# Optimization experiments

Measured on AMD Instinct MI355X. Metric: run time of the kernel, lower is better.

## Reference

```python
import jax, jax.numpy as jnp
import numpy as np

NUM_TOKENS = 100
D_MODEL = 256
NUM_RBF = 50
CUTOFF = 12.0


def setup_inputs() -> dict:
    key = jax.random.key(0)
    k1, k2, k3, k4, k5 = jax.random.split(key, 5)
    B, N = 16, 512
    atomic_numbers = jax.random.randint(k1, (B, N), 0, NUM_TOKENS)
    # scale positions so pairwise distances span [0, cutoff]
    positions = jax.random.normal(k2, (B, N, 3), dtype=jnp.float32) * 3.0
    token_emb = jax.random.normal(k3, (NUM_TOKENS, D_MODEL), dtype=jnp.float32) * 0.02
    proj_w = jax.random.normal(k4, (NUM_RBF, D_MODEL), dtype=jnp.float32) * (1.0 / np.sqrt(NUM_RBF))
    proj_b = jax.random.normal(k5, (D_MODEL,), dtype=jnp.float32) * 0.01
    return {"atomic_numbers": atomic_numbers, "positions": positions,
            "token_emb": token_emb, "proj_w": proj_w, "proj_b": proj_b}


def reference(atomic_numbers, positions, token_emb, proj_w, proj_b):
    # pairwise distances [B, N, N]
    diff = positions[:, :, None, :] - positions[:, None, :, :]
    dist = jnp.sqrt(jnp.sum(diff * diff, axis=-1) + 1e-8)
    # fixed Gaussian RBF expansion [B, N, N, K]
    centers = jnp.linspace(0.0, CUTOFF, NUM_RBF, dtype=jnp.float32)
    width = (centers[1] - centers[0]) * 2.0
    rbf = jnp.exp(-((dist[..., None] - centers) ** 2) / (width * width))
    # mean over neighbor axis -> [B, N, K]
    rbf_mean = jnp.mean(rbf, axis=2)
    rbf_embeddings = rbf_mean @ proj_w + proj_b  # [B, N, d_model]
    token_embeddings = token_emb[atomic_numbers]  # [B, N, d_model]
    return token_embeddings + rbf_embeddings
```

## Files before the change

### kernel.cpp

```cpp
#include <hip/hip_runtime.h>

#define S_C     2.45229158f
#define TWO_DS  1.20112241f

typedef float v2f __attribute__((ext_vector_type(2)));

__device__ __forceinline__ float fast_exp2(float x) {
#if __has_builtin(__builtin_amdgcn_exp2f)
    return __builtin_amdgcn_exp2f(x);
#else
    float r;
    asm("v_exp_f32 %0, %1" : "=v"(r) : "v"(x));
    return r;
#endif
}
__device__ __forceinline__ float fast_sqrt(float x) {
#if __has_builtin(__builtin_amdgcn_sqrtf)
    return __builtin_amdgcn_sqrtf(x);
#else
    return sqrtf(x);
#endif
}

__constant__ const float NEGC[5] = {0.0f, -6.00561204f, -12.0112241f, -18.0168361f, -24.0224482f};
#define E5_1 6.73794700e-3f
#define E5_2 4.53999298e-5f
#define E5_3 3.05902321e-7f
#define E5_4 2.06115362e-9f
#define E10_1 4.53999298e-5f
#define E10_2 2.06115362e-9f
#define E10_3 9.35762297e-14f
#define E10_4 4.24835426e-18f

template <bool FUSED>
__global__ __launch_bounds__(256)
void rbf_mean_kernel(const float* __restrict__ pos,
                     float* __restrict__ meanout,
                     const int* __restrict__ an,
                     const float* __restrict__ te,
                     const float* __restrict__ pw,
                     const float* __restrict__ pb,
                     float* __restrict__ out)
{
    __shared__ v2f red2[4][32 * 25];
    __shared__ float ms[4][52];

    const int w    = threadIdx.x >> 6;
    const int lane = threadIdx.x & 63;
    const int row  = blockIdx.x * 4 + w;
    const int b    = row >> 9;
    const int i    = row & 511;

    const float* posb = pos + (size_t)b * 512 * 3;

    float jx[8], jy[8], jz[8];
#pragma unroll
    for (int jj = 0; jj < 8; ++jj) {
        const int j = jj * 64 + lane;
        jx[jj] = posb[j * 3 + 0];
        jy[jj] = posb[j * 3 + 1];
        jz[jj] = posb[j * 3 + 2];
    }
    const float pix = posb[i * 3 + 0];
    const float piy = posb[i * 3 + 1];
    const float piz = posb[i * 3 + 2];

    v2f acc[25];
#pragma unroll
    for (int m = 0; m < 25; ++m) acc[m] = (v2f){0.0f, 0.0f};

#pragma unroll
    for (int jj = 0; jj < 8; ++jj) {
        const float dx = pix - jx[jj];
        const float dy = piy - jy[jj];
        const float dz = piz - jz[jj];
        const float d2 = fmaf(dx, dx, fmaf(dy, dy, fmaf(dz, dz, 1e-8f)));
        float dS = fast_sqrt(d2) * S_C;
        dS = fminf(dS, 42.0f);
        const float Ap = fast_exp2(dS * TWO_DS);
        const float A  = Ap * Ap;

#pragma unroll
        for (int c = 0; c < 5; ++c) {
            const float u  = dS + NEGC[c];
            const float t0 = fast_exp2(-(u * u));
            const float Ac  = (c == 0) ? Ap :
                              (c == 1) ? Ap * E5_1 :
                              (c == 2) ? Ap * E5_2 :
                              (c == 3) ? Ap * E5_3 : Ap * E5_4;
            const float Ac2 = (c == 0) ? A :
                              (c == 1) ? A * E10_1 :
                              (c == 2) ? A * E10_2 :
                              (c == 3) ? A * E10_3 : A * E10_4;
            v2f g = {t0, t0 * Ac};
            acc[5 * c + 0] += g;
            const v2f M = {Ac2, Ac2};
#pragma unroll
            for (int t = 1; t < 5; ++t) {
                g = g * M;
                acc[5 * c + t] += g;
            }
        }
    }

    {
        const v2f QP[5] = {{1.0f,            0.778800783f},
                           {0.367879441f,    0.105399225f},
                           {1.83156389e-2f,  1.93045414e-3f},
                           {1.23409804e-4f,  4.78511739e-6f},
                           {1.12535175e-7f,  1.60522806e-9f}};
#pragma unroll
        for (int m = 0; m < 25; ++m) acc[m] = acc[m] * QP[m % 5];
    }

#pragma unroll
    for (int m = 0; m < 25; ++m) {
        const float lx = __shfl_xor(acc[m].x, 1);
        const float ly = __shfl_xor(acc[m].y, 1);
        acc[m] += (v2f){lx, ly};
    }
    if ((lane & 1) == 0) {
        v2f* myrow = &red2[w][(lane >> 1) * 25];
#pragma unroll
        for (int m = 0; m < 25; ++m) myrow[m] = acc[m];
    }
    __syncthreads();

    float meanv = 0.0f;
    if (lane < 50) {
        const float* col = (const float*)&red2[w][0] + lane;
        float s0 = 0.f, s1 = 0.f, s2 = 0.f, s3 = 0.f;
#pragma unroll
        for (int r = 0; r < 32; r += 4) {
            s0 += col[(r + 0) * 50];
            s1 += col[(r + 1) * 50];
            s2 += col[(r + 2) * 50];
            s3 += col[(r + 3) * 50];
        }
        meanv = ((s0 + s1) + (s2 + s3)) * (1.0f / 512.0f);
    }

    if (!FUSED) {
        if (lane < 50) meanout[(size_t)row * 50 + lane] = meanv;
        return;
    }

    if (lane < 50) ms[w][lane] = meanv;
    __syncthreads();

    const int tok = an[row];
    float4 o = reinterpret_cast<const float4*>(pb)[lane];
    const float4 t = reinterpret_cast<const float4*>(te + (size_t)tok * 256)[lane];
    o.x += t.x; o.y += t.y; o.z += t.z; o.w += t.w;
#pragma unroll
    for (int k = 0; k < 50; ++k) {
        const float mk = ms[w][k];
        const float4 w4 = reinterpret_cast<const float4*>(pw + k * 256)[lane];
        o.x = fmaf(mk, w4.x, o.x);
        o.y = fmaf(mk, w4.y, o.y);
        o.z = fmaf(mk, w4.z, o.z);
        o.w = fmaf(mk, w4.w, o.w);
    }
    reinterpret_cast<float4*>(out)[(size_t)row * 64 + lane] = o;
}

__global__ __launch_bounds__(256)
void proj_kernel(const float* __restrict__ mean,
                 const int* __restrict__ an,
                 const float* __restrict__ te,
                 const float* __restrict__ pw,
                 const float* __restrict__ pb,
                 float* __restrict__ out)
{
    const int w    = threadIdx.x >> 6;
    const int lane = threadIdx.x & 63;
    int wid = blockIdx.x * 4 + w;
    wid = __builtin_amdgcn_readfirstlane(wid);
    const int row0 = wid * 4;

    const float4 bias = reinterpret_cast<const float4*>(pb)[lane];
    float4 o[4];
#pragma unroll
    for (int r = 0; r < 4; ++r) {
        const int tok = an[row0 + r];
        const float4 t = reinterpret_cast<const float4*>(te + (size_t)tok * 256)[lane];
        o[r].x = bias.x + t.x; o[r].y = bias.y + t.y;
        o[r].z = bias.z + t.z; o[r].w = bias.w + t.w;
    }
#pragma unroll
    for (int k = 0; k < 50; ++k) {
        const float4 w4 = reinterpret_cast<const float4*>(pw + (size_t)k * 256)[lane];
#pragma unroll
        for (int r = 0; r < 4; ++r) {
            const float mk = mean[(size_t)(row0 + r) * 50 + k];
            o[r].x = fmaf(mk, w4.x, o[r].x);
            o[r].y = fmaf(mk, w4.y, o[r].y);
            o[r].z = fmaf(mk, w4.z, o[r].z);
            o[r].w = fmaf(mk, w4.w, o[r].w);
        }
    }
#pragma unroll
    for (int r = 0; r < 4; ++r)
        reinterpret_cast<float4*>(out)[(size_t)(row0 + r) * 64 + lane] = o[r];
}

extern "C" void kernel_launch(void* const* d_in, const int* in_sizes, int n_in,
                              void* d_out, int out_size, void* d_ws, size_t ws_size,
                              hipStream_t stream)
{
    const int*   an  = (const int*)  d_in[0];
    const float* pos = (const float*)d_in[1];
    const float* te  = (const float*)d_in[2];
    const float* pw  = (const float*)d_in[3];
    const float* pb  = (const float*)d_in[4];
    float* out = (float*)d_out;

    const size_t mean_bytes = (size_t)8192 * 50 * sizeof(float);
    if (ws_size >= mean_bytes) {
        float* mean = (float*)d_ws;
        rbf_mean_kernel<false><<<2048, 256, 0, stream>>>(pos, mean, nullptr, nullptr,
                                                         nullptr, nullptr, nullptr);
        proj_kernel<<<512, 256, 0, stream>>>(mean, an, te, pw, pb, out);
    } else {
        rbf_mean_kernel<true><<<2048, 256, 0, stream>>>(pos, nullptr, an, te, pw, pb, out);
    }
}
```

Before: 26.64 us.

## Always run single fused RBF-mean and projection kernel, drop block barriers

Removes the two-kernel path, where means were written to workspace and a separate projection kernel read them back, and always launches one fused kernel that does the RBF mean and the projection together. This avoids a second launch and the global-memory round trip for the means. The cost is that the projection weights are reloaded for every row instead of being shared across four rows. Both __syncthreads are removed because each wave only uses its own shared-memory slice, which relies on wavefront lockstep for LDS ordering. The constant-memory NEGC table and the squared-exponent constants are replaced with inline arithmetic.

```diff
diff --git a/kernel.cpp b/kernel.cpp
--- a/kernel.cpp
+++ b/kernel.cpp
@@ -2,6 +2,11 @@
 
 #define S_C     2.45229158f
 #define TWO_DS  1.20112241f
+#define TEN_D   6.00560980f
+#define E5_1 6.73794700e-3f
+#define E5_2 4.53999298e-5f
+#define E5_3 3.05902321e-7f
+#define E5_4 2.06115362e-9f
 
 typedef float v2f __attribute__((ext_vector_type(2)));
 
@@ -22,27 +27,15 @@
 #endif
 }
 
-__constant__ const float NEGC[5] = {0.0f, -6.00561204f, -12.0112241f, -18.0168361f, -24.0224482f};
-#define E5_1 6.73794700e-3f
-#define E5_2 4.53999298e-5f
-#define E5_3 3.05902321e-7f
-#define E5_4 2.06115362e-9f
-#define E10_1 4.53999298e-5f
-#define E10_2 2.06115362e-9f
-#define E10_3 9.35762297e-14f
-#define E10_4 4.24835426e-18f
-
-template <bool FUSED>
 __global__ __launch_bounds__(256)
-void rbf_mean_kernel(const float* __restrict__ pos,
-                     float* __restrict__ meanout,
-                     const int* __restrict__ an,
-                     const float* __restrict__ te,
-                     const float* __restrict__ pw,
-                     const float* __restrict__ pb,
-                     float* __restrict__ out)
+void rbf_fused_kernel(const float* __restrict__ pos,
+                      const int* __restrict__ an,
+                      const float* __restrict__ te,
+                      const float* __restrict__ pw,
+                      const float* __restrict__ pb,
+                      float* __restrict__ out)
 {
-    __shared__ v2f red2[4][32 * 25];
+    __shared__ v2f   red2[4][32 * 25];
     __shared__ float ms[4][52];
 
     const int w    = threadIdx.x >> 6;
@@ -51,7 +44,7 @@
     const int b    = row >> 9;
     const int i    = row & 511;
 
-    const float* posb = pos + (size_t)b * 512 * 3;
+    const float* posb = pos + (size_t)b * 1536;
 
     float jx[8], jy[8], jz[8];
 #pragma unroll
@@ -78,20 +71,16 @@
         float dS = fast_sqrt(d2) * S_C;
         dS = fminf(dS, 42.0f);
         const float Ap = fast_exp2(dS * TWO_DS);
-        const float A  = Ap * Ap;
 
 #pragma unroll
         for (int c = 0; c < 5; ++c) {
-            const float u  = dS + NEGC[c];
+            const float u  = dS - (float)c * TEN_D;
             const float t0 = fast_exp2(-(u * u));
             const float Ac  = (c == 0) ? Ap :
                               (c == 1) ? Ap * E5_1 :
                               (c == 2) ? Ap * E5_2 :
                               (c == 3) ? Ap * E5_3 : Ap * E5_4;
-            const float Ac2 = (c == 0) ? A :
-                              (c == 1) ? A * E10_1 :
-                              (c == 2) ? A * E10_2 :
-                              (c == 3) ? A * E10_3 : A * E10_4;
+            const float Ac2 = Ac * Ac;
             v2f g = {t0, t0 * Ac};
             acc[5 * c + 0] += g;
             const v2f M = {Ac2, Ac2};
@@ -124,9 +113,7 @@
 #pragma unroll
         for (int m = 0; m < 25; ++m) myrow[m] = acc[m];
     }
-    __syncthreads();
 
-    float meanv = 0.0f;
     if (lane < 50) {
         const float* col = (const float*)&red2[w][0] + lane;
         float s0 = 0.f, s1 = 0.f, s2 = 0.f, s3 = 0.f;
@@ -137,16 +124,8 @@
             s2 += col[(r + 2) * 50];
             s3 += col[(r + 3) * 50];
         }
-        meanv = ((s0 + s1) + (s2 + s3)) * (1.0f / 512.0f);
+        ms[w][lane] = ((s0 + s1) + (s2 + s3)) * (1.0f / 512.0f);
     }
-
-    if (!FUSED) {
-        if (lane < 50) meanout[(size_t)row * 50 + lane] = meanv;
-        return;
-    }
-
-    if (lane < 50) ms[w][lane] = meanv;
-    __syncthreads();
 
     const int tok = an[row];
     float4 o = reinterpret_cast<const float4*>(pb)[lane];
@@ -164,46 +143,6 @@
     reinterpret_cast<float4*>(out)[(size_t)row * 64 + lane] = o;
 }
 
-__global__ __launch_bounds__(256)
-void proj_kernel(const float* __restrict__ mean,
-                 const int* __restrict__ an,
-                 const float* __restrict__ te,
-                 const float* __restrict__ pw,
-                 const float* __restrict__ pb,
-                 float* __restrict__ out)
-{
-    const int w    = threadIdx.x >> 6;
-    const int lane = threadIdx.x & 63;
-    int wid = blockIdx.x * 4 + w;
-    wid = __builtin_amdgcn_readfirstlane(wid);
-    const int row0 = wid * 4;
-
-    const float4 bias = reinterpret_cast<const float4*>(pb)[lane];
-    float4 o[4];
-#pragma unroll
-    for (int r = 0; r < 4; ++r) {
-        const int tok = an[row0 + r];
-        const float4 t = reinterpret_cast<const float4*>(te + (size_t)tok * 256)[lane];
-        o[r].x = bias.x + t.x; o[r].y = bias.y + t.y;
-        o[r].z = bias.z + t.z; o[r].w = bias.w + t.w;
-    }
-#pragma unroll
-    for (int k = 0; k < 50; ++k) {
-        const float4 w4 = reinterpret_cast<const float4*>(pw + (size_t)k * 256)[lane];
-#pragma unroll
-        for (int r = 0; r < 4; ++r) {
-            const float mk = mean[(size_t)(row0 + r) * 50 + k];
-            o[r].x = fmaf(mk, w4.x, o[r].x);
-            o[r].y = fmaf(mk, w4.y, o[r].y);
-            o[r].z = fmaf(mk, w4.z, o[r].z);
-            o[r].w = fmaf(mk, w4.w, o[r].w);
-        }
-    }
-#pragma unroll
-    for (int r = 0; r < 4; ++r)
-        reinterpret_cast<float4*>(out)[(size_t)(row0 + r) * 64 + lane] = o[r];
-}
-
 extern "C" void kernel_launch(void* const* d_in, const int* in_sizes, int n_in,
                               void* d_out, int out_size, void* d_ws, size_t ws_size,
                               hipStream_t stream)
@@ -215,13 +154,5 @@
     const float* pb  = (const float*)d_in[4];
     float* out = (float*)d_out;
 
-    const size_t mean_bytes = (size_t)8192 * 50 * sizeof(float);
-    if (ws_size >= mean_bytes) {
-        float* mean = (float*)d_ws;
-        rbf_mean_kernel<false><<<2048, 256, 0, stream>>>(pos, mean, nullptr, nullptr,
-                                                         nullptr, nullptr, nullptr);
-        proj_kernel<<<512, 256, 0, stream>>>(mean, an, te, pw, pb, out);
-    } else {
-        rbf_mean_kernel<true><<<2048, 256, 0, stream>>>(pos, nullptr, an, te, pw, pb, out);
-    }
+    rbf_fused_kernel<<<2048, 256, 0, stream>>>(pos, an, te, pw, pb, out);
 }
```

After: 27.31 us. +2.5%, slower.
